# Performance work log

Hardware: AMD Instinct MI355X
Metric: run time of the kernel (lower is better)

## Reference

```python
import jax, jax.numpy as jnp
import numpy as np

H = 2048          # hidden_size
NH = 16           # num_heads
HD = H // NH      # head_dim = 128
B, S = 2, 2048


def setup_inputs() -> dict:
    key = jax.random.key(0)
    ks = jax.random.split(key, 9)
    sc_h = 1.0 / np.sqrt(H)
    x = jax.random.normal(ks[0], (B, S, H), dtype=jnp.float32)
    # torch nn.Linear weights are [out_features, in_features]
    Wq = jax.random.uniform(ks[1], (H, H), jnp.float32, -sc_h, sc_h)
    bq = jax.random.uniform(ks[2], (H,), jnp.float32, -sc_h, sc_h)
    Wk = jax.random.uniform(ks[3], (HD, H), jnp.float32, -sc_h, sc_h)
    bk = jax.random.uniform(ks[4], (HD,), jnp.float32, -sc_h, sc_h)
    Wv = jax.random.uniform(ks[5], (HD, H), jnp.float32, -sc_h, sc_h)
    bv = jax.random.uniform(ks[6], (HD,), jnp.float32, -sc_h, sc_h)
    Wo = jax.random.uniform(ks[7], (H, H), jnp.float32, -sc_h, sc_h)
    bo = jax.random.uniform(ks[8], (H,), jnp.float32, -sc_h, sc_h)
    return {"x": x, "Wq": Wq, "bq": bq, "Wk": Wk, "bk": bk,
            "Wv": Wv, "bv": bv, "Wo": Wo, "bo": bo}


def reference(x, Wq, bq, Wk, bk, Wv, bv, Wo, bo):
    b, s, _ = x.shape
    q = (jnp.einsum('bsh,oh->bso', x, Wq) + bq).reshape(b, s, NH, HD)
    q = q.transpose(0, 2, 1, 3)                      # [b, nh, s, hd]
    k = jnp.einsum('bsh,dh->bsd', x, Wk) + bk        # [b, s, hd] single KV head
    v = jnp.einsum('bsh,dh->bsd', x, Wv) + bv
    # shared-K attention scores: broadcast single K head across query heads
    attn = jnp.einsum('bnsd,btd->bnst', q, k) / jnp.sqrt(jnp.float32(HD))
    attn = jax.nn.softmax(attn, axis=-1)
    out = jnp.einsum('bnst,btd->bnsd', attn, v)      # [b, nh, s, hd]
    out = out.transpose(0, 2, 1, 3).reshape(b, s, H)
    return jnp.einsum('bsh,oh->bso', out, Wo) + bo
```

## Files before the change

kernel.cpp:

```cpp
#include <hip/hip_runtime.h>
#include <hip/hip_bf16.h>

typedef unsigned short u16;
typedef __bf16 bf16x8 __attribute__((ext_vector_type(8)));
typedef float f32x4 __attribute__((ext_vector_type(4)));

#define AS1 __attribute__((address_space(1)))
#define AS3 __attribute__((address_space(3)))

__device__ __forceinline__ u16 f2bf(float f) {
  unsigned u = __builtin_bit_cast(unsigned, f);
  u += 0x7FFFu + ((u >> 16) & 1u);
  return (u16)(u >> 16);
}

__device__ __forceinline__ void gload_lds16(const void* g, void* l) {
  __builtin_amdgcn_global_load_lds((AS1 void*)g, (AS3 void*)l, 16, 0, 0);
}

__global__ __launch_bounds__(256) void cvt_bf16(const float* __restrict__ in,
                                                u16* __restrict__ out, int n,
                                                float scale) {
  int i = (blockIdx.x * 256 + threadIdx.x) * 8;
  if (i >= n) return;
  float4 a = *(const float4*)(in + i);
  float4 b = *(const float4*)(in + i + 4);
  u16 t[8] = {f2bf(a.x * scale), f2bf(a.y * scale), f2bf(a.z * scale), f2bf(a.w * scale),
              f2bf(b.x * scale), f2bf(b.y * scale), f2bf(b.z * scale), f2bf(b.w * scale)};
  *(uint4*)(out + i) = *(const uint4*)t;
}

__global__ __launch_bounds__(256)
void cvt_weights(const float* __restrict__ Wq, const float* __restrict__ Wk,
                 const float* __restrict__ Wv, const float* __restrict__ Wo,
                 const float* __restrict__ bq, const float* __restrict__ bk,
                 const float* __restrict__ bv,
                 u16* __restrict__ wqkv, u16* __restrict__ wo,
                 float* __restrict__ bias_a, float qs) {
  const long NQ = 524288, NK = 32768, NV = 32768, NO = 524288;
  const long NW = NQ + NK + NV + NO;
  long i = (long)blockIdx.x * 256 + threadIdx.x;
  if (i >= NW) {
    int t = (int)(i - NW);
    if (t < 2048) bias_a[t] = bq[t] * qs;
    else if (t < 2176) bias_a[t] = bk[t - 2048];
    else if (t < 2304) bias_a[t] = bv[t - 2176];
    return;
  }
  const float* src;
  u16* dst;
  float s = 1.f;
  if (i < NQ) { src = Wq + i * 8; dst = wqkv + i * 8; s = qs; }
  else if (i < NQ + NK) { long j = i - NQ; src = Wk + j * 8; dst = wqkv + 2048l * 2048 + j * 8; }
  else if (i < NQ + NK + NV) { long j = i - NQ - NK; src = Wv + j * 8; dst = wqkv + 2176l * 2048 + j * 8; }
  else { long j = i - NQ - NK - NV; src = Wo + j * 8; dst = wo + j * 8; }
  float4 a = *(const float4*)src;
  float4 b = *(const float4*)(src + 4);
  u16 t[8] = {f2bf(a.x * s), f2bf(a.y * s), f2bf(a.z * s), f2bf(a.w * s),
              f2bf(b.x * s), f2bf(b.y * s), f2bf(b.z * s), f2bf(b.w * s)};
  *(uint4*)dst = *(const uint4*)t;
}

template<int MODE>
__global__ __launch_bounds__(256)
void gemm_bt(const u16* __restrict__ A, const u16* __restrict__ B,
             const float* __restrict__ bias, void* __restrict__ C0,
             void* __restrict__ C1, void* __restrict__ C2,
             int M, int N, int K, float scale)
{
  __shared__ u16 As[128 * 32];
  __shared__ u16 Bs[128 * 32];
  const int tid = threadIdx.x;
  const int wave = tid >> 6, lane = tid & 63;
  const int g = lane >> 4, r = lane & 15;
  const int wrow = (wave >> 1) * 64, wcol = (wave & 1) * 64;

  const int gx = gridDim.x;
  int lin = blockIdx.y * gx + blockIdx.x;
  const int cpx = (gx * gridDim.y) >> 3;
  lin = (lin & 7) * cpx + (lin >> 3);
  const long tM = (long)(lin / gx) * 128, tN = (long)(lin % gx) * 128;

  const int r0 = wave * 16 + (lane >> 2);
  const int c0 = (lane & 3) * 8;

  f32x4 acc[4][4] = {};
  char* As3 = (char*)As;
  char* Bs3 = (char*)Bs;

  for (int kt = 0; kt < K; kt += 32) {
    __syncthreads();
    const u16* gA = A + (tM + r0) * K + kt + c0;
    const u16* gB = B + (tN + r0) * K + kt + c0;
    gload_lds16(gA,                As3 + wave * 1024);
    gload_lds16(gA + (long)64 * K, As3 + 4096 + wave * 1024);
    gload_lds16(gB,                Bs3 + wave * 1024);
    gload_lds16(gB + (long)64 * K, Bs3 + 4096 + wave * 1024);
    __syncthreads();

    bf16x8 a[4], b[4];
#pragma unroll
    for (int m = 0; m < 4; m++)
      a[m] = *(const bf16x8*)(As + (wrow + m * 16 + r) * 32 + g * 8);
#pragma unroll
    for (int n = 0; n < 4; n++)
      b[n] = *(const bf16x8*)(Bs + (wcol + n * 16 + r) * 32 + g * 8);
#pragma unroll
    for (int m = 0; m < 4; m++)
#pragma unroll
      for (int n = 0; n < 4; n++)
        acc[m][n] = __builtin_amdgcn_mfma_f32_16x16x32_bf16(a[m], b[n], acc[m][n], 0, 0, 0);
  }

#pragma unroll
  for (int m = 0; m < 4; m++) {
    const long row0 = tM + wrow + m * 16 + g * 4;
#pragma unroll
    for (int n = 0; n < 4; n++) {
      const long col = tN + wcol + n * 16 + r;
      const float bb = bias[col];
      if (MODE == 0) {
#pragma unroll
        for (int q = 0; q < 4; q++)
          ((float*)C0)[(row0 + q) * N + col] = (acc[m][n][q] + bb) * scale;
      } else {
        u16 vals[4];
#pragma unroll
        for (int q = 0; q < 4; q++) vals[q] = f2bf(acc[m][n][q] + bb);
        if (col < 2048) {
#pragma unroll
          for (int q = 0; q < 4; q++)
            ((u16*)C0)[(row0 + q) * 2048 + col] = vals[q];
        } else if (col < 2176) {
#pragma unroll
          for (int q = 0; q < 4; q++)
            ((u16*)C1)[(row0 + q) * 128 + (col - 2048)] = vals[q];
        } else {
          const long b2 = row0 >> 11;
          const long t0r = row0 & 2047;
          const int tl = (int)(t0r & 63);
          const int rbase = tl & 15, blk = tl >> 4;
          u16* vp = (u16*)C2 + (b2 * 128 + (col - 2176)) * 2048 + (t0r >> 6) * 64;
#pragma unroll
          for (int q = 0; q < 4; q++)
            vp[(rbase + q) * 4 + blk] = vals[q];
        }
      }
    }
  }
}

__global__ __launch_bounds__(256, 2)
void attn_mqa11(const u16* __restrict__ Q, const u16* __restrict__ Kb,
                const u16* __restrict__ VT, u16* __restrict__ O)
{
  constexpr int S = 2048;
  const int bid = blockIdx.x;
  const int qt = bid & 15;
  const int head = (bid >> 4) & 15;
  const int b = bid >> 8;
  const int tid = threadIdx.x;
  const int wave = tid >> 6, lane = tid & 63;
  const int g = lane >> 4, r = lane & 15;

  __shared__ u16 Ks[2][64 * 128];
  __shared__ u16 VTs[2][128 * 64];
  __shared__ u16 Ps[4][16 * 64];

  bf16x8 qf[2][4];
#pragma unroll
  for (int qb = 0; qb < 2; qb++) {
    const u16* qp = Q + (long)(b * S + qt * 128 + qb * 64 + wave * 16 + r) * 2048
                      + head * 128 + g * 8;
#pragma unroll
    for (int ks = 0; ks < 4; ks++) qf[qb][ks] = *(const bf16x8*)(qp + ks * 32);
  }

  f32x4 oacc[2][8] = {};
  float lsum[2][4] = {};
  char* psb = (char*)Ps[wave];

  auto stageK = [&](int buf, int t0) {
    char* dst = (char*)Ks[buf];
#pragma unroll
    for (int p = 0; p < 4; p++) {
      int D = p * 4096 + wave * 1024 + lane * 16;
      int row = D >> 8;
      int col2 = (D & 255) ^ ((row & 7) << 4);
      gload_lds16(Kb + ((long)b * S + t0 + row) * 128 + (col2 >> 1), dst + D);
    }
  };
  auto stageV = [&](int buf, int t0) {
    char* dst = (char*)VTs[buf];
#pragma unroll
    for (int p = 0; p < 4; p++) {
      int D = p * 4096 + wave * 1024 + lane * 16;
      int row = D >> 7;
      int colb = (D & 127) ^ ((row & 7) << 4);
      gload_lds16(VT + ((long)b * 128 + row) * 2048 + t0 + (colb >> 1), dst + D);
    }
  };

  stageK(0, 0);
  stageV(0, 0);
  __syncthreads();

  for (int t0 = 0; t0 < S; t0 += 64) {
    const int cur = (t0 >> 6) & 1;
    const bool nxt = (t0 + 64) < S;

    if (nxt) { stageK(cur ^ 1, t0 + 64); stageV(cur ^ 1, t0 + 64); }

    char* Ks3 = (char*)Ks[cur];
    f32x4 st[2][4] = {};
#pragma unroll
    for (int ks = 0; ks < 4; ks++) {
#pragma unroll
      for (int nf = 0; nf < 4; nf++) {
        const int trow = nf * 16 + r;
        const int col2 = (ks * 64 + g * 16) ^ ((trow & 7) << 4);
        bf16x8 kf = *(const bf16x8*)(Ks3 + trow * 256 + col2);
        st[0][nf] = __builtin_amdgcn_mfma_f32_16x16x32_bf16(qf[0][ks], kf, st[0][nf], 0, 0, 0);
        st[1][nf] = __builtin_amdgcn_mfma_f32_16x16x32_bf16(qf[1][ks], kf, st[1][nf], 0, 0, 0);
      }
    }

    char* Vs3 = (char*)VTs[cur];
    bf16x8 vreg[2][8];
#pragma unroll
    for (int qb = 0; qb < 2; qb++) {
#pragma unroll
      for (int q = 0; q < 4; q++) {
        const int prow = g * 4 + q;
        u16 pk[4];
#pragma unroll
        for (int nf = 0; nf < 4; nf++) {
          float p = exp2f(st[qb][nf][q]);
          lsum[qb][q] += p;
          pk[nf] = __builtin_bit_cast(u16, (__bf16)p);
        }
        *(ushort4*)(psb + prow * 128 + ((r * 8) ^ ((prow & 7) << 4))) =
            *(const ushort4*)pk;
      }
#pragma unroll
      for (int ks = 0; ks < 2; ks++) {
        bf16x8 pf = *(const bf16x8*)(psb + r * 128 +
                                     ((ks * 64 + g * 16) ^ ((r & 7) << 4)));
#pragma unroll
        for (int dn = 0; dn < 8; dn++) {
          if (qb == 0) {
            const int d = dn * 16 + r;
            vreg[ks][dn] = *(const bf16x8*)(Vs3 + d * 128 +
                                            ((ks * 64 + g * 16) ^ ((d & 7) << 4)));
          }
          oacc[qb][dn] = __builtin_amdgcn_mfma_f32_16x16x32_bf16(pf, vreg[ks][dn],
                                                                 oacc[qb][dn], 0, 0, 0);
        }
      }
    }

    __syncthreads();
  }

#pragma unroll
  for (int off = 1; off < 16; off <<= 1)
#pragma unroll
    for (int qb = 0; qb < 2; qb++)
#pragma unroll
      for (int q = 0; q < 4; q++)
        lsum[qb][q] += __shfl_xor(lsum[qb][q], off);

#pragma unroll
  for (int qb = 0; qb < 2; qb++) {
#pragma unroll
    for (int q = 0; q < 4; q++) {
      const float inv = 1.f / lsum[qb][q];
      const long orow = (long)(b * S + qt * 128 + qb * 64 + wave * 16 + g * 4 + q);
#pragma unroll
      for (int dn = 0; dn < 8; dn++)
        O[orow * 2048 + head * 128 + dn * 16 + r] = f2bf(oacc[qb][dn][q] * inv);
    }
  }
}

extern "C" void kernel_launch(void* const* d_in, const int* in_sizes, int n_in,
                              void* d_out, int out_size, void* d_ws, size_t ws_size,
                              hipStream_t stream) {
  const float* x  = (const float*)d_in[0];
  const float* Wq = (const float*)d_in[1];
  const float* bq = (const float*)d_in[2];
  const float* Wk = (const float*)d_in[3];
  const float* bk = (const float*)d_in[4];
  const float* Wv = (const float*)d_in[5];
  const float* bv = (const float*)d_in[6];
  const float* Wo = (const float*)d_in[7];
  const float* bo = (const float*)d_in[8];
  float* out = (float*)d_out;

  char* ws = (char*)d_ws;
  u16* x_bf     = (u16*)(ws + (0ul  << 20));
  u16* q_bf     = (u16*)(ws + (16ul << 20));
  u16* wqkv_bf  = (u16*)(ws + (32ul << 20));
  u16* wo_bf    = (u16*)(ws + (42ul << 20));
  u16* k_bf     = (u16*)(ws + (50ul << 20));
  u16* vt_bf    = (u16*)(ws + (51ul << 20));
  u16* attn_bf  = (u16*)(ws + (52ul << 20));
  float* bias_a = (float*)(ws + (68ul << 20));

  const int BS = 4096, H = 2048;
  const float QS = 0.12751744f;

  cvt_bf16<<<BS * H / 8 / 256, 256, 0, stream>>>(x, x_bf, BS * H, 1.f);
  cvt_weights<<<4361, 256, 0, stream>>>(Wq, Wk, Wv, Wo, bq, bk, bv,
                                        wqkv_bf, wo_bf, bias_a, QS);

  gemm_bt<3><<<dim3(18, 32), 256, 0, stream>>>(
      x_bf, wqkv_bf, bias_a, q_bf, k_bf, vt_bf, 4096, 2304, 2048, 1.0f);
  attn_mqa11<<<512, 256, 0, stream>>>(q_bf, k_bf, vt_bf, attn_bf);
  gemm_bt<0><<<dim3(16, 32), 256, 0, stream>>>(
      attn_bf, wo_bf, bo, out, nullptr, nullptr, 4096, 2048, 2048, 1.0f);
}
```

Baseline: 224.5 us.

## Merge conversion kernels, add MFMA wave priority, use native exp2 in attention

The separate activation and weight fp32-to-bf16 conversion kernels become a single launch that covers x, the four weight matrices and the biases, saving one kernel launch and its tail. In the attention kernel, s_setprio raises wave priority around the QK and PV MFMA blocks so matrix work is favoured over softmax and load waves. exp2f is replaced with the hardware exp2 builtin to drop range-handling instructions. The builtin may be less exact for denormal or extreme inputs, and the priority hints depend on how the scheduler interleaves waves.

```diff
diff --git a/kernel.cpp b/kernel.cpp
--- a/kernel.cpp
+++ b/kernel.cpp
@@ -18,27 +18,16 @@
   __builtin_amdgcn_global_load_lds((AS1 void*)g, (AS3 void*)l, 16, 0, 0);
 }
 
-__global__ __launch_bounds__(256) void cvt_bf16(const float* __restrict__ in,
-                                                u16* __restrict__ out, int n,
-                                                float scale) {
-  int i = (blockIdx.x * 256 + threadIdx.x) * 8;
-  if (i >= n) return;
-  float4 a = *(const float4*)(in + i);
-  float4 b = *(const float4*)(in + i + 4);
-  u16 t[8] = {f2bf(a.x * scale), f2bf(a.y * scale), f2bf(a.z * scale), f2bf(a.w * scale),
-              f2bf(b.x * scale), f2bf(b.y * scale), f2bf(b.z * scale), f2bf(b.w * scale)};
-  *(uint4*)(out + i) = *(const uint4*)t;
-}
-
 __global__ __launch_bounds__(256)
-void cvt_weights(const float* __restrict__ Wq, const float* __restrict__ Wk,
-                 const float* __restrict__ Wv, const float* __restrict__ Wo,
-                 const float* __restrict__ bq, const float* __restrict__ bk,
-                 const float* __restrict__ bv,
-                 u16* __restrict__ wqkv, u16* __restrict__ wo,
-                 float* __restrict__ bias_a, float qs) {
-  const long NQ = 524288, NK = 32768, NV = 32768, NO = 524288;
-  const long NW = NQ + NK + NV + NO;
+void cvt_all(const float* __restrict__ x,
+             const float* __restrict__ Wq, const float* __restrict__ Wk,
+             const float* __restrict__ Wv, const float* __restrict__ Wo,
+             const float* __restrict__ bq, const float* __restrict__ bk,
+             const float* __restrict__ bv,
+             u16* __restrict__ xb, u16* __restrict__ wqkv, u16* __restrict__ wo,
+             float* __restrict__ bias_a, float qs) {
+  const long NX = 1048576, NQ = 524288, NK = 32768, NV = 32768, NO = 524288;
+  const long NW = NX + NQ + NK + NV + NO;
   long i = (long)blockIdx.x * 256 + threadIdx.x;
   if (i >= NW) {
     int t = (int)(i - NW);
@@ -50,10 +39,11 @@
   const float* src;
   u16* dst;
   float s = 1.f;
-  if (i < NQ) { src = Wq + i * 8; dst = wqkv + i * 8; s = qs; }
-  else if (i < NQ + NK) { long j = i - NQ; src = Wk + j * 8; dst = wqkv + 2048l * 2048 + j * 8; }
-  else if (i < NQ + NK + NV) { long j = i - NQ - NK; src = Wv + j * 8; dst = wqkv + 2176l * 2048 + j * 8; }
-  else { long j = i - NQ - NK - NV; src = Wo + j * 8; dst = wo + j * 8; }
+  if (i < NX) { src = x + i * 8; dst = xb + i * 8; }
+  else if (i < NX + NQ) { long j = i - NX; src = Wq + j * 8; dst = wqkv + j * 8; s = qs; }
+  else if (i < NX + NQ + NK) { long j = i - NX - NQ; src = Wk + j * 8; dst = wqkv + 2048l * 2048 + j * 8; }
+  else if (i < NX + NQ + NK + NV) { long j = i - NX - NQ - NK; src = Wv + j * 8; dst = wqkv + 2176l * 2048 + j * 8; }
+  else { long j = i - NX - NQ - NK - NV; src = Wo + j * 8; dst = wo + j * 8; }
   float4 a = *(const float4*)src;
   float4 b = *(const float4*)(src + 4);
   u16 t[8] = {f2bf(a.x * s), f2bf(a.y * s), f2bf(a.z * s), f2bf(a.w * s),
@@ -151,7 +141,7 @@
 }
 
 __global__ __launch_bounds__(256, 2)
-void attn_mqa11(const u16* __restrict__ Q, const u16* __restrict__ Kb,
+void attn_mqa12(const u16* __restrict__ Q, const u16* __restrict__ Kb,
                 const u16* __restrict__ VT, u16* __restrict__ O)
 {
   constexpr int S = 2048;
@@ -213,6 +203,7 @@
 
     char* Ks3 = (char*)Ks[cur];
     f32x4 st[2][4] = {};
+    __builtin_amdgcn_s_setprio(1);
 #pragma unroll
     for (int ks = 0; ks < 4; ks++) {
 #pragma unroll
@@ -224,6 +215,7 @@
         st[1][nf] = __builtin_amdgcn_mfma_f32_16x16x32_bf16(qf[1][ks], kf, st[1][nf], 0, 0, 0);
       }
     }
+    __builtin_amdgcn_s_setprio(0);
 
     char* Vs3 = (char*)VTs[cur];
     bf16x8 vreg[2][8];
@@ -235,13 +227,14 @@
         u16 pk[4];
 #pragma unroll
         for (int nf = 0; nf < 4; nf++) {
-          float p = exp2f(st[qb][nf][q]);
+          float p = __builtin_amdgcn_exp2f(st[qb][nf][q]);
           lsum[qb][q] += p;
           pk[nf] = __builtin_bit_cast(u16, (__bf16)p);
         }
         *(ushort4*)(psb + prow * 128 + ((r * 8) ^ ((prow & 7) << 4))) =
             *(const ushort4*)pk;
       }
+      __builtin_amdgcn_s_setprio(1);
 #pragma unroll
       for (int ks = 0; ks < 2; ks++) {
         bf16x8 pf = *(const bf16x8*)(psb + r * 128 +
@@ -257,6 +250,7 @@
                                                                  oacc[qb][dn], 0, 0, 0);
         }
       }
+      __builtin_amdgcn_s_setprio(0);
     }
 
     __syncthreads();
@@ -307,16 +301,14 @@
   u16* attn_bf  = (u16*)(ws + (52ul << 20));
   float* bias_a = (float*)(ws + (68ul << 20));
 
-  const int BS = 4096, H = 2048;
   const float QS = 0.12751744f;
 
-  cvt_bf16<<<BS * H / 8 / 256, 256, 0, stream>>>(x, x_bf, BS * H, 1.f);
-  cvt_weights<<<4361, 256, 0, stream>>>(Wq, Wk, Wv, Wo, bq, bk, bv,
-                                        wqkv_bf, wo_bf, bias_a, QS);
+  cvt_all<<<8457, 256, 0, stream>>>(x, Wq, Wk, Wv, Wo, bq, bk, bv,
+                                    x_bf, wqkv_bf, wo_bf, bias_a, QS);
 
   gemm_bt<3><<<dim3(18, 32), 256, 0, stream>>>(
       x_bf, wqkv_bf, bias_a, q_bf, k_bf, vt_bf, 4096, 2304, 2048, 1.0f);
-  attn_mqa11<<<512, 256, 0, stream>>>(q_bf, k_bf, vt_bf, attn_bf);
+  attn_mqa12<<<512, 256, 0, stream>>>(q_bf, k_bf, vt_bf, attn_bf);
   gemm_bt<0><<<dim3(16, 32), 256, 0, stream>>>(
       attn_bf, wo_bf, bo, out, nullptr, nullptr, 4096, 2048, 2048, 1.0f);
 }
```

After: 209.8 us. 6.6% less time.
